# Performance work log

Hardware: AMD Instinct MI355X
Metric: run time of the kernel (lower is better)

The kernel has to match this reference:

```python
import math
import jax, jax.numpy as jnp
import numpy as np

CHUNK_LEN = 64
NUM_HEADS = 16
HIDDEN = 1024
HEAD = HIDDEN // NUM_HEADS


def setup_inputs() -> dict:
    key = jax.random.key(0)
    ks = jax.random.split(key, 8)
    B, S, C, N, L = 4, 2048, 32, 2, 128
    scale = 1.0 / math.sqrt(HIDDEN)
    return {
        "query": jax.random.normal(ks[0], (B, S, HIDDEN), jnp.float32),
        "kv": jax.random.normal(ks[1], (B, C, N, L, HIDDEN), jnp.float32),
        "Wq": jax.random.normal(ks[2], (HIDDEN, HIDDEN), jnp.float32) * scale,
        "bq": jnp.zeros((HIDDEN,), jnp.float32),
        "Wk": jax.random.normal(ks[3], (HIDDEN, HIDDEN), jnp.float32) * scale,
        "bk": jnp.zeros((HIDDEN,), jnp.float32),
        "Wv": jax.random.normal(ks[4], (HIDDEN, HIDDEN), jnp.float32) * scale,
        "bv": jnp.zeros((HIDDEN,), jnp.float32),
    }


def reference(query, kv, Wq, bq, Wk, bk, Wv, bv):
    B, S, H = query.shape
    _, C, N, L, _ = kv.shape
    # shift query right by chunk_len-1 and pad to n_chunks*chunk_len
    q = query[:, CHUNK_LEN - 1:]
    add_len = C * CHUNK_LEN - q.shape[1]
    q = jnp.pad(q, ((0, 0), (0, add_len), (0, 0)))
    q = q.reshape(B, C, CHUNK_LEN, H)
    q = (q @ Wq.T + bq).reshape(B, C, CHUNK_LEN, NUM_HEADS, HEAD)
    k = (kv @ Wk.T + bk).reshape(B, C, N, L, NUM_HEADS, HEAD)
    v = (kv @ Wv.T + bv).reshape(B, C, N, L, NUM_HEADS, HEAD)
    # scores: [B, C, heads, chunk_len, N, L]
    attn = jnp.einsum("bcihd,bcnjhd->bchinj", q, k) / math.sqrt(HEAD)
    # softmax over flattened neighbor dims (n, j)
    attn = jax.nn.softmax(attn.reshape(B, C, NUM_HEADS, CHUNK_LEN, N * L), axis=-1)
    attn = attn.reshape(B, C, NUM_HEADS, CHUNK_LEN, N, L)
    h = jnp.einsum("bchinj,bcnjhd->bcihd", attn, v).reshape(B, C * CHUNK_LEN, H)
    # shift left: prepend chunk_len-1 zeros, truncate to seq_len
    h = jnp.pad(h, ((0, 0), (CHUNK_LEN - 1, 0), (0, 0)))[:, :S]
    return h
```

## Files before the change

### kernel.cpp

```cpp
#include <hip/hip_runtime.h>
#include <stdint.h>

#define HD 1024
#define SEQ 2048
#define NC 32

typedef __bf16 bf16x4 __attribute__((ext_vector_type(4)));
typedef __bf16 bf16x8 __attribute__((ext_vector_type(8)));
typedef float f32x4 __attribute__((ext_vector_type(4)));

__device__ inline unsigned short f2bf(float f) {
  union { float f; unsigned int u; } v; v.f = f;
  unsigned int r = v.u + 0x7fffu + ((v.u >> 16) & 1u);
  return (unsigned short)(r >> 16);
}
__device__ inline unsigned int pk2bf(float a, float b) {
  return (unsigned int)f2bf(a) | ((unsigned int)f2bf(b) << 16);
}
__device__ inline bf16x8 ld_frag8(const unsigned short* p) {
  bf16x4 lo = *(const bf16x4*)p;
  bf16x4 hi = *(const bf16x4*)(p + 4);
  return __builtin_shufflevector(lo, hi, 0, 1, 2, 3, 4, 5, 6, 7);
}
__device__ inline void glds16(const unsigned short* g, unsigned short* l) {
  __builtin_amdgcn_global_load_lds(
      (const __attribute__((address_space(1))) unsigned int*)g,
      (__attribute__((address_space(3))) unsigned int*)l, 16, 0, 0);
}
__device__ inline int2 swz_bid() {
  int lin = blockIdx.y * 8 + blockIdx.x;
  int s = (lin & 7) * (int)gridDim.y + (lin >> 3);
  return make_int2(s & 7, s >> 3);
}

__global__ __launch_bounds__(256) void zero_head_kernel(float* __restrict__ out) {
  int i = (blockIdx.x * 256 + threadIdx.x) * 4;
  int b = i / 64512;
  int r = i - b * 64512;
  *(float4*)(out + (size_t)b * (SEQ * HD) + r) = make_float4(0.f, 0.f, 0.f, 0.f);
}

__global__ __launch_bounds__(256) void cvt_kernel(const float* __restrict__ in,
                                                  unsigned short* __restrict__ out, int n8) {
  int i = blockIdx.x * 256 + threadIdx.x;
  if (i < n8) {
    float4 a = ((const float4*)in)[(size_t)i * 2];
    float4 b = ((const float4*)in)[(size_t)i * 2 + 1];
    ((uint4*)out)[i] = make_uint4(pk2bf(a.x, a.y), pk2bf(a.z, a.w),
                                  pk2bf(b.x, b.y), pk2bf(b.z, b.w));
  }
}

__global__ __launch_bounds__(256) void cvt_q_kernel(const float* __restrict__ q,
                                                    unsigned short* __restrict__ out) {
  int i = blockIdx.x * 256 + threadIdx.x;
  int g = i >> 7, c8 = (i & 127) * 8;
  int b = g >> 11, tt = g & 2047;
  uint4 o = make_uint4(0, 0, 0, 0);
  if (tt < 1985) {
    const float* src = q + ((size_t)(b << 11) + tt + 63) * HD + c8;
    float4 a = *(const float4*)src;
    float4 bb = *(const float4*)(src + 4);
    o = make_uint4(pk2bf(a.x, a.y), pk2bf(a.z, a.w), pk2bf(bb.x, bb.y), pk2bf(bb.z, bb.w));
  }
  *(uint4*)(out + (size_t)g * HD + c8) = o;
}

__global__ __launch_bounds__(256, 2) void gemm_bf_kernel(
    const unsigned short* __restrict__ A, const unsigned short* __restrict__ W,
    const float* __restrict__ bias, unsigned short* __restrict__ Cout, int store_vt) {
  __shared__ unsigned short lds_a[128 * 32];
  __shared__ unsigned short lds_b[128 * 32];
  const int t = threadIdx.x;
  const int l = t & 63, w = t >> 6;
  const int wm = w >> 1, wn = w & 1;
  const int lr = l & 15, lq = l >> 4;
  const int2 bid = swz_bid();
  const size_t arow0 = (size_t)bid.y * 128;
  const size_t brow0 = (size_t)bid.x * 128;
  const int c0 = t, c1 = 256 + t;
  const unsigned short* a0 = A + (arow0 + (c0 >> 2)) * HD + (c0 & 3) * 8;
  const unsigned short* a1 = A + (arow0 + (c1 >> 2)) * HD + (c1 & 3) * 8;
  const unsigned short* b0 = W + (brow0 + (c0 >> 2)) * HD + (c0 & 3) * 8;
  const unsigned short* b1 = W + (brow0 + (c1 >> 2)) * HD + (c1 & 3) * 8;

  f32x4 acc[4][4];
  for (int i = 0; i < 4; i++)
    for (int j = 0; j < 4; j++) acc[i][j] = (f32x4){0.f, 0.f, 0.f, 0.f};

  for (int kk = 0; kk < 32; ++kk) {
    const int k0 = kk * 32;
    __syncthreads();
    glds16(a0 + k0, lds_a + c0 * 8);
    glds16(a1 + k0, lds_a + c1 * 8);
    glds16(b0 + k0, lds_b + c0 * 8);
    glds16(b1 + k0, lds_b + c1 * 8);
    __syncthreads();
    bf16x8 af[4], bfr[4];
    for (int mt = 0; mt < 4; ++mt)
      af[mt] = *(const bf16x8*)(lds_a + (wm * 64 + mt * 16 + lr) * 32 + lq * 8);
    for (int nt = 0; nt < 4; ++nt)
      bfr[nt] = *(const bf16x8*)(lds_b + (wn * 64 + nt * 16 + lr) * 32 + lq * 8);
    for (int mt = 0; mt < 4; ++mt)
      for (int nt = 0; nt < 4; ++nt)
        acc[mt][nt] = __builtin_amdgcn_mfma_f32_16x16x32_bf16(af[mt], bfr[nt], acc[mt][nt], 0, 0, 0);
  }

  if (!store_vt) {
    for (int nt = 0; nt < 4; ++nt) {
      int n = bid.x * 128 + wn * 64 + nt * 16 + lr;
      float bvv = bias[n];
      for (int mt = 0; mt < 4; ++mt) {
        size_t mbase = arow0 + wm * 64 + mt * 16 + lq * 4;
        for (int r = 0; r < 4; ++r)
          Cout[(mbase + r) * HD + n] = f2bf(acc[mt][nt][r] + bvv);
      }
    }
  } else {
    for (int nt = 0; nt < 4; ++nt) {
      int n = bid.x * 128 + wn * 64 + nt * 16 + lr;
      float bvv = bias[n];
      int h = n >> 6, d = n & 63;
      for (int mt = 0; mt < 4; ++mt) {
        size_t m0 = arow0 + wm * 64 + mt * 16 + lq * 4;
        size_t bc = m0 >> 8, j = m0 & 255;
        *(ushort4*)(Cout + ((bc * 16 + h) * 64 + d) * 256 + j) =
            make_ushort4(f2bf(acc[mt][nt][0] + bvv), f2bf(acc[mt][nt][1] + bvv),
                         f2bf(acc[mt][nt][2] + bvv), f2bf(acc[mt][nt][3] + bvv));
      }
    }
  }
}

__global__ __launch_bounds__(256, 2) void gemm_kv_kernel(
    const unsigned short* __restrict__ A, const unsigned short* __restrict__ Wk,
    const unsigned short* __restrict__ Wv, const float* __restrict__ bk,
    const float* __restrict__ bv, unsigned short* __restrict__ Kout,
    unsigned short* __restrict__ Vt) {
  __shared__ unsigned short lds_a[128 * 32];
  __shared__ unsigned short lds_k[128 * 32];
  __shared__ unsigned short lds_v[128 * 32];
  const int t = threadIdx.x;
  const int l = t & 63, w = t >> 6;
  const int wm = w >> 1, wn = w & 1;
  const int lr = l & 15, lq = l >> 4;
  const int2 bid = swz_bid();
  const size_t arow0 = (size_t)bid.y * 128;
  const size_t brow0 = (size_t)bid.x * 128;
  const int c0 = t, c1 = 256 + t;
  const unsigned short* a0 = A + (arow0 + (c0 >> 2)) * HD + (c0 & 3) * 8;
  const unsigned short* a1 = A + (arow0 + (c1 >> 2)) * HD + (c1 & 3) * 8;
  const unsigned short* k0p = Wk + (brow0 + (c0 >> 2)) * HD + (c0 & 3) * 8;
  const unsigned short* k1p = Wk + (brow0 + (c1 >> 2)) * HD + (c1 & 3) * 8;
  const unsigned short* v0p = Wv + (brow0 + (c0 >> 2)) * HD + (c0 & 3) * 8;
  const unsigned short* v1p = Wv + (brow0 + (c1 >> 2)) * HD + (c1 & 3) * 8;

  f32x4 acck[4][4], accv[4][4];
  for (int i = 0; i < 4; i++)
    for (int j = 0; j < 4; j++) {
      acck[i][j] = (f32x4){0.f, 0.f, 0.f, 0.f};
      accv[i][j] = (f32x4){0.f, 0.f, 0.f, 0.f};
    }

  for (int kk = 0; kk < 32; ++kk) {
    const int k0 = kk * 32;
    __syncthreads();
    glds16(a0 + k0, lds_a + c0 * 8);
    glds16(a1 + k0, lds_a + c1 * 8);
    glds16(k0p + k0, lds_k + c0 * 8);
    glds16(k1p + k0, lds_k + c1 * 8);
    glds16(v0p + k0, lds_v + c0 * 8);
    glds16(v1p + k0, lds_v + c1 * 8);
    __syncthreads();
    bf16x8 af[4];
    for (int mt = 0; mt < 4; ++mt)
      af[mt] = *(const bf16x8*)(lds_a + (wm * 64 + mt * 16 + lr) * 32 + lq * 8);
    {
      bf16x8 bfr[4];
      for (int nt = 0; nt < 4; ++nt)
        bfr[nt] = *(const bf16x8*)(lds_k + (wn * 64 + nt * 16 + lr) * 32 + lq * 8);
      for (int mt = 0; mt < 4; ++mt)
        for (int nt = 0; nt < 4; ++nt)
          acck[mt][nt] = __builtin_amdgcn_mfma_f32_16x16x32_bf16(af[mt], bfr[nt], acck[mt][nt], 0, 0, 0);
    }
    {
      bf16x8 bfr[4];
      for (int nt = 0; nt < 4; ++nt)
        bfr[nt] = *(const bf16x8*)(lds_v + (wn * 64 + nt * 16 + lr) * 32 + lq * 8);
      for (int mt = 0; mt < 4; ++mt)
        for (int nt = 0; nt < 4; ++nt)
          accv[mt][nt] = __builtin_amdgcn_mfma_f32_16x16x32_bf16(af[mt], bfr[nt], accv[mt][nt], 0, 0, 0);
    }
  }

  for (int nt = 0; nt < 4; ++nt) {
    int n = bid.x * 128 + wn * 64 + nt * 16 + lr;
    float bvv = bk[n];
    for (int mt = 0; mt < 4; ++mt) {
      size_t mbase = arow0 + wm * 64 + mt * 16 + lq * 4;
      for (int r = 0; r < 4; ++r)
        Kout[(mbase + r) * HD + n] = f2bf(acck[mt][nt][r] + bvv);
    }
  }
  for (int nt = 0; nt < 4; ++nt) {
    int n = bid.x * 128 + wn * 64 + nt * 16 + lr;
    float bvv = bv[n];
    int h = n >> 6, d = n & 63;
    for (int mt = 0; mt < 4; ++mt) {
      size_t m0 = arow0 + wm * 64 + mt * 16 + lq * 4;
      size_t bc = m0 >> 8, j = m0 & 255;
      *(ushort4*)(Vt + ((bc * 16 + h) * 64 + d) * 256 + j) =
          make_ushort4(f2bf(accv[mt][nt][0] + bvv), f2bf(accv[mt][nt][1] + bvv),
                       f2bf(accv[mt][nt][2] + bvv), f2bf(accv[mt][nt][3] + bvv));
    }
  }
}

__global__ __launch_bounds__(256, 2) void gemm_f32_kernel(
    const float* __restrict__ A, const float* __restrict__ W,
    const float* __restrict__ bias, unsigned short* __restrict__ Cout,
    int store_vt, int qremap) {
  __shared__ unsigned short lds_a[128 * 32];
  __shared__ unsigned short lds_b[128 * 32];
  const int t = threadIdx.x;
  const int l = t & 63, w = t >> 6;
  const int wm = w >> 1, wn = w & 1;
  const int lr = l & 15, lq = l >> 4;
  const size_t arow0 = (size_t)blockIdx.y * 128;
  const size_t brow0 = (size_t)blockIdx.x * 128;

  f32x4 acc[4][4];
  for (int i = 0; i < 4; i++)
    for (int j = 0; j < 4; j++) acc[i][j] = (f32x4){0.f, 0.f, 0.f, 0.f};

  for (int kk = 0; kk < 32; ++kk) {
    const int k0 = kk * 32;
    uint4 av[2], bv[2];
    for (int p = 0; p < 2; ++p) {
      int chunk = p * 256 + t;
      int row = chunk >> 2, c8 = (chunk & 3) * 8;
      size_t grow = arow0 + row;
      bool valid = true;
      const float* srcA;
      if (qremap) {
        int bb = (int)(grow >> 11), tt = (int)(grow & 2047);
        valid = tt < 1985;
        srcA = A + ((size_t)(bb << 11) + tt + 63) * HD + k0 + c8;
      } else {
        srcA = A + grow * HD + k0 + c8;
      }
      if (valid) {
        float4 x = *(const float4*)srcA, y = *(const float4*)(srcA + 4);
        av[p] = make_uint4(pk2bf(x.x, x.y), pk2bf(x.z, x.w), pk2bf(y.x, y.y), pk2bf(y.z, y.w));
      } else av[p] = make_uint4(0, 0, 0, 0);
      const float* srcB = W + (brow0 + row) * HD + k0 + c8;
      float4 x = *(const float4*)srcB, y = *(const float4*)(srcB + 4);
      bv[p] = make_uint4(pk2bf(x.x, x.y), pk2bf(x.z, x.w), pk2bf(y.x, y.y), pk2bf(y.z, y.w));
    }
    __syncthreads();
    for (int p = 0; p < 2; ++p) {
      int chunk = p * 256 + t;
      *(uint4*)(lds_a + chunk * 8) = av[p];
      *(uint4*)(lds_b + chunk * 8) = bv[p];
    }
    __syncthreads();
    bf16x8 af[4], bfr[4];
    for (int mt = 0; mt < 4; ++mt)
      af[mt] = *(const bf16x8*)(lds_a + (wm * 64 + mt * 16 + lr) * 32 + lq * 8);
    for (int nt = 0; nt < 4; ++nt)
      bfr[nt] = *(const bf16x8*)(lds_b + (wn * 64 + nt * 16 + lr) * 32 + lq * 8);
    for (int mt = 0; mt < 4; ++mt)
      for (int nt = 0; nt < 4; ++nt)
        acc[mt][nt] = __builtin_amdgcn_mfma_f32_16x16x32_bf16(af[mt], bfr[nt], acc[mt][nt], 0, 0, 0);
  }

  if (!store_vt) {
    for (int nt = 0; nt < 4; ++nt) {
      int n = blockIdx.x * 128 + wn * 64 + nt * 16 + lr;
      float bvv = bias[n];
      for (int mt = 0; mt < 4; ++mt) {
        size_t mbase = arow0 + wm * 64 + mt * 16 + lq * 4;
        for (int r = 0; r < 4; ++r)
          Cout[(mbase + r) * HD + n] = f2bf(acc[mt][nt][r] + bvv);
      }
    }
  } else {
    for (int nt = 0; nt < 4; ++nt) {
      int n = blockIdx.x * 128 + wn * 64 + nt * 16 + lr;
      float bvv = bias[n];
      int h = n >> 6, d = n & 63;
      for (int mt = 0; mt < 4; ++mt) {
        size_t m0 = arow0 + wm * 64 + mt * 16 + lq * 4;
        size_t bc = m0 >> 8, j = m0 & 255;
        *(ushort4*)(Cout + ((bc * 16 + h) * 64 + d) * 256 + j) =
            make_ushort4(f2bf(acc[mt][nt][0] + bvv), f2bf(acc[mt][nt][1] + bvv),
                         f2bf(acc[mt][nt][2] + bvv), f2bf(acc[mt][nt][3] + bvv));
      }
    }
  }
}

#define QK_STRIDE 68
#define P_STRIDE 260

__global__ __launch_bounds__(256, 3) void attn_kernel(
    const unsigned short* __restrict__ Qp, const unsigned short* __restrict__ Kp,
    const unsigned short* __restrict__ Vt, float* __restrict__ out) {
  __shared__ unsigned short q_s[64 * QK_STRIDE];
  __shared__ unsigned short k_s[256 * QK_STRIDE];
  const int t = threadIdx.x;
  const int l = t & 63, w = t >> 6;
  const int lr = l & 15, lq = l >> 4;
  const int bid = blockIdx.x;
  const int head = bid & 15, cc = (bid >> 4) & 31, b = bid >> 9;
  const size_t qrow0 = (size_t)(b * NC + cc) * 64;
  const size_t kvrow0 = (size_t)(b * NC + cc) * 256;
  const int hcol = head * 64;
  const unsigned short* vbase = Vt + ((size_t)((b * NC + cc) * 16 + head) * 64) * 256;

  for (int p = 0; p < 4; ++p) {
    int chunk = p * 256 + t;
    int row = chunk >> 4, c4 = (chunk & 15) * 4;
    *(uint2*)(q_s + row * QK_STRIDE + c4) = *(const uint2*)(Qp + (qrow0 + row) * HD + hcol + c4);
  }
  for (int p = 0; p < 16; ++p) {
    int chunk = p * 256 + t;
    int row = chunk >> 4, c4 = (chunk & 15) * 4;
    *(uint2*)(k_s + row * QK_STRIDE + c4) = *(const uint2*)(Kp + (kvrow0 + row) * HD + hcol + c4);
  }
  __syncthreads();

  bf16x8 qa0 = ld_frag8(q_s + (w * 16 + lr) * QK_STRIDE + lq * 8);
  bf16x8 qa1 = ld_frag8(q_s + (w * 16 + lr) * QK_STRIDE + 32 + lq * 8);
  f32x4 sc[16];
  for (int nt = 0; nt < 16; ++nt) {
    bf16x8 kb0 = ld_frag8(k_s + (nt * 16 + lr) * QK_STRIDE + lq * 8);
    bf16x8 kb1 = ld_frag8(k_s + (nt * 16 + lr) * QK_STRIDE + 32 + lq * 8);
    f32x4 a = (f32x4){0.f, 0.f, 0.f, 0.f};
    a = __builtin_amdgcn_mfma_f32_16x16x32_bf16(qa0, kb0, a, 0, 0, 0);
    a = __builtin_amdgcn_mfma_f32_16x16x32_bf16(qa1, kb1, a, 0, 0, 0);
    sc[nt] = a;
  }
  float mrow[4] = {-1e30f, -1e30f, -1e30f, -1e30f};
  for (int nt = 0; nt < 16; ++nt)
    for (int r = 0; r < 4; ++r) mrow[r] = fmaxf(mrow[r], sc[nt][r]);
  for (int off = 1; off < 16; off <<= 1)
    for (int r = 0; r < 4; ++r) mrow[r] = fmaxf(mrow[r], __shfl_xor(mrow[r], off, 16));
  float srow[4] = {0.f, 0.f, 0.f, 0.f};
  const float cexp = 0.18033688011112042f;
  for (int nt = 0; nt < 16; ++nt)
    for (int r = 0; r < 4; ++r) {
      float p = exp2f((sc[nt][r] - mrow[r]) * cexp);
      sc[nt][r] = p;
      srow[r] += p;
    }
  for (int off = 1; off < 16; off <<= 1)
    for (int r = 0; r < 4; ++r) srow[r] += __shfl_xor(srow[r], off, 16);

  __syncthreads();

  for (int nt = 0; nt < 16; ++nt)
    for (int r = 0; r < 4; ++r)
      k_s[(w * 16 + lq * 4 + r) * P_STRIDE + nt * 16 + lr] = f2bf(sc[nt][r]);

  f32x4 o[4];
  for (int i = 0; i < 4; ++i) o[i] = (f32x4){0.f, 0.f, 0.f, 0.f};
  for (int ks = 0; ks < 8; ++ks) {
    bf16x8 pa = ld_frag8(k_s + (w * 16 + lr) * P_STRIDE + ks * 32 + lq * 8);
    for (int nt2 = 0; nt2 < 4; ++nt2) {
      bf16x8 vb = *(const bf16x8*)(vbase + (size_t)(nt2 * 16 + lr) * 256 + ks * 32 + lq * 8);
      o[nt2] = __builtin_amdgcn_mfma_f32_16x16x32_bf16(pa, vb, o[nt2], 0, 0, 0);
    }
  }

  for (int r = 0; r < 4; ++r) {
    int strip = w * 16 + lq * 4 + r;
    int trow = cc * 64 + strip;
    if (trow < 1985) {
      size_t orow = (size_t)b * SEQ + trow + 63;
      float inv = 1.0f / srow[r];
      for (int nt2 = 0; nt2 < 4; ++nt2)
        out[orow * HD + hcol + nt2 * 16 + lr] = o[nt2][r] * inv;
    }
  }
}

extern "C" void kernel_launch(void* const* d_in, const int* in_sizes, int n_in,
                              void* d_out, int out_size, void* d_ws, size_t ws_size,
                              hipStream_t stream) {
  (void)in_sizes; (void)n_in; (void)out_size;
  const float* query = (const float*)d_in[0];
  const float* kv    = (const float*)d_in[1];
  const float* Wq    = (const float*)d_in[2];
  const float* bq    = (const float*)d_in[3];
  const float* Wk    = (const float*)d_in[4];
  const float* bk    = (const float*)d_in[5];
  const float* Wv    = (const float*)d_in[6];
  const float* bv    = (const float*)d_in[7];
  float* out = (float*)d_out;

  unsigned short* Qp  = (unsigned short*)d_ws;
  unsigned short* Kp  = Qp + (size_t)8192 * 1024;
  unsigned short* Vt  = Kp + (size_t)32768 * 1024;
  unsigned short* Qbf = Vt + (size_t)32768 * 1024;
  unsigned short* KVb = Qbf + (size_t)8192 * 1024;
  unsigned short* Wqb = KVb + (size_t)32768 * 1024;
  unsigned short* Wkb = Wqb + (size_t)1024 * 1024;
  unsigned short* Wvb = Wkb + (size_t)1024 * 1024;
  const size_t need = ((size_t)8192 * 1024 * 2 + (size_t)32768 * 1024 * 2 + (size_t)1024 * 1024 * 3) * 2;
  const bool big = ws_size >= need;

  zero_head_kernel<<<dim3(252), dim3(256), 0, stream>>>(out);
  if (big) {
    cvt_q_kernel<<<dim3(4096), dim3(256), 0, stream>>>(query, Qbf);
    cvt_kernel<<<dim3(16384), dim3(256), 0, stream>>>(kv, KVb, 4194304);
    cvt_kernel<<<dim3(512), dim3(256), 0, stream>>>(Wq, Wqb, 131072);
    cvt_kernel<<<dim3(512), dim3(256), 0, stream>>>(Wk, Wkb, 131072);
    cvt_kernel<<<dim3(512), dim3(256), 0, stream>>>(Wv, Wvb, 131072);
    gemm_bf_kernel<<<dim3(8, 64), dim3(256), 0, stream>>>(Qbf, Wqb, bq, Qp, 0);
    gemm_kv_kernel<<<dim3(8, 256), dim3(256), 0, stream>>>(KVb, Wkb, Wvb, bk, bv, Kp, Vt);
  } else {
    gemm_f32_kernel<<<dim3(8, 64), dim3(256), 0, stream>>>(query, Wq, bq, Qp, 0, 1);
    gemm_f32_kernel<<<dim3(8, 256), dim3(256), 0, stream>>>(kv, Wk, bk, Kp, 0, 0);
    gemm_f32_kernel<<<dim3(8, 256), dim3(256), 0, stream>>>(kv, Wv, bv, Vt, 1, 0);
  }
  attn_kernel<<<dim3(2048), dim3(256), 0, stream>>>(Qp, Kp, Vt, out);
}
```

Measured before the change: 484.4 us.

## Double-buffer GEMMs, swizzle LDS, fuse kv conversion into KV GEMM, widen attn loads

Both projection GEMMs now double-buffer their LDS tiles, so the next K-slice is loaded while MFMAs run on the current one, with one barrier per iteration instead of two. The LDS layout is XOR-swizzled to avoid bank conflicts on fragment reads. The KV GEMM reads fp32 kv directly and converts it to bf16 in registers before writing LDS, which removes the separate kv conversion pass and its large intermediate buffer. The attention kernel loads Q/K with 16-byte vectors and a padded stride of 72. The cost is double the LDS and more registers, which may lower occupancy.

```diff
diff --git a/kernel.cpp b/kernel.cpp
--- a/kernel.cpp
+++ b/kernel.cpp
@@ -31,6 +31,13 @@
   int lin = blockIdx.y * 8 + blockIdx.x;
   int s = (lin & 7) * (int)gridDim.y + (lin >> 3);
   return make_int2(s & 7, s >> 3);
+}
+__device__ inline int inv_swz(int pc) {
+  int b2 = (pc >> 2) & 1, b3 = (pc >> 3) & 1, b4 = (pc >> 4) & 1;
+  return pc ^ (b2 ^ b4) ^ (b3 << 1) ^ (b4 << 2);
+}
+__device__ inline int swz_rd(int row, int lq) {
+  return (((row << 2) | lq) ^ (row & 7)) << 3;
 }
 
 __global__ __launch_bounds__(256) void zero_head_kernel(float* __restrict__ out) {
@@ -66,11 +73,11 @@
   *(uint4*)(out + (size_t)g * HD + c8) = o;
 }
 
-__global__ __launch_bounds__(256, 2) void gemm_bf_kernel(
+__global__ __launch_bounds__(256, 2) void gemm_q_kernel(
     const unsigned short* __restrict__ A, const unsigned short* __restrict__ W,
-    const float* __restrict__ bias, unsigned short* __restrict__ Cout, int store_vt) {
-  __shared__ unsigned short lds_a[128 * 32];
-  __shared__ unsigned short lds_b[128 * 32];
+    const float* __restrict__ bias, unsigned short* __restrict__ Cout) {
+  __shared__ unsigned short lds_a[2][4096];
+  __shared__ unsigned short lds_b[2][4096];
   const int t = threadIdx.x;
   const int l = t & 63, w = t >> 6;
   const int wm = w >> 1, wn = w & 1;
@@ -78,68 +85,62 @@
   const int2 bid = swz_bid();
   const size_t arow0 = (size_t)bid.y * 128;
   const size_t brow0 = (size_t)bid.x * 128;
-  const int c0 = t, c1 = 256 + t;
-  const unsigned short* a0 = A + (arow0 + (c0 >> 2)) * HD + (c0 & 3) * 8;
-  const unsigned short* a1 = A + (arow0 + (c1 >> 2)) * HD + (c1 & 3) * 8;
-  const unsigned short* b0 = W + (brow0 + (c0 >> 2)) * HD + (c0 & 3) * 8;
-  const unsigned short* b1 = W + (brow0 + (c1 >> 2)) * HD + (c1 & 3) * 8;
+  const int lc = inv_swz(t);
+  const int r0 = lc >> 2, c8 = (lc & 3) * 8;
+  const unsigned short* a0 = A + (arow0 + r0) * HD + c8;
+  const unsigned short* a1 = a0 + 64 * HD;
+  const unsigned short* b0 = W + (brow0 + r0) * HD + c8;
+  const unsigned short* b1 = b0 + 64 * HD;
 
   f32x4 acc[4][4];
   for (int i = 0; i < 4; i++)
     for (int j = 0; j < 4; j++) acc[i][j] = (f32x4){0.f, 0.f, 0.f, 0.f};
 
-  for (int kk = 0; kk < 32; ++kk) {
-    const int k0 = kk * 32;
-    __syncthreads();
-    glds16(a0 + k0, lds_a + c0 * 8);
-    glds16(a1 + k0, lds_a + c1 * 8);
-    glds16(b0 + k0, lds_b + c0 * 8);
-    glds16(b1 + k0, lds_b + c1 * 8);
-    __syncthreads();
+  auto stage = [&](int buf, int k0) {
+    glds16(a0 + k0, lds_a[buf] + t * 8);
+    glds16(a1 + k0, lds_a[buf] + 2048 + t * 8);
+    glds16(b0 + k0, lds_b[buf] + t * 8);
+    glds16(b1 + k0, lds_b[buf] + 2048 + t * 8);
+  };
+  auto compute = [&](int buf) {
     bf16x8 af[4], bfr[4];
     for (int mt = 0; mt < 4; ++mt)
-      af[mt] = *(const bf16x8*)(lds_a + (wm * 64 + mt * 16 + lr) * 32 + lq * 8);
+      af[mt] = *(const bf16x8*)(lds_a[buf] + swz_rd(wm * 64 + mt * 16 + lr, lq));
     for (int nt = 0; nt < 4; ++nt)
-      bfr[nt] = *(const bf16x8*)(lds_b + (wn * 64 + nt * 16 + lr) * 32 + lq * 8);
+      bfr[nt] = *(const bf16x8*)(lds_b[buf] + swz_rd(wn * 64 + nt * 16 + lr, lq));
     for (int mt = 0; mt < 4; ++mt)
       for (int nt = 0; nt < 4; ++nt)
         acc[mt][nt] = __builtin_amdgcn_mfma_f32_16x16x32_bf16(af[mt], bfr[nt], acc[mt][nt], 0, 0, 0);
-  }
-
-  if (!store_vt) {
-    for (int nt = 0; nt < 4; ++nt) {
-      int n = bid.x * 128 + wn * 64 + nt * 16 + lr;
-      float bvv = bias[n];
-      for (int mt = 0; mt < 4; ++mt) {
-        size_t mbase = arow0 + wm * 64 + mt * 16 + lq * 4;
-        for (int r = 0; r < 4; ++r)
-          Cout[(mbase + r) * HD + n] = f2bf(acc[mt][nt][r] + bvv);
-      }
-    }
-  } else {
-    for (int nt = 0; nt < 4; ++nt) {
-      int n = bid.x * 128 + wn * 64 + nt * 16 + lr;
-      float bvv = bias[n];
-      int h = n >> 6, d = n & 63;
-      for (int mt = 0; mt < 4; ++mt) {
-        size_t m0 = arow0 + wm * 64 + mt * 16 + lq * 4;
-        size_t bc = m0 >> 8, j = m0 & 255;
-        *(ushort4*)(Cout + ((bc * 16 + h) * 64 + d) * 256 + j) =
-            make_ushort4(f2bf(acc[mt][nt][0] + bvv), f2bf(acc[mt][nt][1] + bvv),
-                         f2bf(acc[mt][nt][2] + bvv), f2bf(acc[mt][nt][3] + bvv));
-      }
+  };
+
+  stage(0, 0);
+  __syncthreads();
+  for (int kk = 0; kk < 31; ++kk) {
+    stage((kk & 1) ^ 1, (kk + 1) * 32);
+    compute(kk & 1);
+    __syncthreads();
+  }
+  compute(1);
+
+  for (int nt = 0; nt < 4; ++nt) {
+    int n = bid.x * 128 + wn * 64 + nt * 16 + lr;
+    float bvv = bias[n];
+    for (int mt = 0; mt < 4; ++mt) {
+      size_t mbase = arow0 + wm * 64 + mt * 16 + lq * 4;
+      for (int r = 0; r < 4; ++r)
+        Cout[(mbase + r) * HD + n] = f2bf(acc[mt][nt][r] + bvv);
     }
   }
 }
 
 __global__ __launch_bounds__(256, 2) void gemm_kv_kernel(
-    const unsigned short* __restrict__ A, const unsigned short* __restrict__ Wk,
+    const float* __restrict__ A, const unsigned short* __restrict__ Wk,
     const unsigned short* __restrict__ Wv, const float* __restrict__ bk,
     const float* __restrict__ bv, unsigned short* __restrict__ Kout,
     unsigned short* __restrict__ Vt) {
-  __shared__ unsigned short lds_a[128 * 32];
-  __shared__ unsigned short lds_k[128 * 32];
-  __shared__ unsigned short lds_v[128 * 32];
+  __shared__ unsigned short lds_a[2][4096];
+  __shared__ unsigned short lds_k[2][4096];
+  __shared__ unsigned short lds_v[2][4096];
   const int t = threadIdx.x;
   const int l = t & 63, w = t >> 6;
   const int wm = w >> 1, wn = w & 1;
@@ -147,13 +148,14 @@
   const int2 bid = swz_bid();
   const size_t arow0 = (size_t)bid.y * 128;
   const size_t brow0 = (size_t)bid.x * 128;
-  const int c0 = t, c1 = 256 + t;
-  const unsigned short* a0 = A + (arow0 + (c0 >> 2)) * HD + (c0 & 3) * 8;
-  const unsigned short* a1 = A + (arow0 + (c1 >> 2)) * HD + (c1 & 3) * 8;
-  const unsigned short* k0p = Wk + (brow0 + (c0 >> 2)) * HD + (c0 & 3) * 8;
-  const unsigned short* k1p = Wk + (brow0 + (c1 >> 2)) * HD + (c1 & 3) * 8;
-  const unsigned short* v0p = Wv + (brow0 + (c0 >> 2)) * HD + (c0 & 3) * 8;
-  const unsigned short* v1p = Wv + (brow0 + (c1 >> 2)) * HD + (c1 & 3) * 8;
+  const int lc = inv_swz(t);
+  const int r0 = lc >> 2, c8 = (lc & 3) * 8;
+  const float* aF0 = A + (arow0 + r0) * HD + c8;
+  const float* aF1 = aF0 + (size_t)64 * HD;
+  const unsigned short* kp0 = Wk + (brow0 + r0) * HD + c8;
+  const unsigned short* kp1 = kp0 + 64 * HD;
+  const unsigned short* vp0 = Wv + (brow0 + r0) * HD + c8;
+  const unsigned short* vp1 = vp0 + 64 * HD;
 
   f32x4 acck[4][4], accv[4][4];
   for (int i = 0; i < 4; i++)
@@ -162,23 +164,31 @@
       accv[i][j] = (f32x4){0.f, 0.f, 0.f, 0.f};
     }
 
-  for (int kk = 0; kk < 32; ++kk) {
-    const int k0 = kk * 32;
-    __syncthreads();
-    glds16(a0 + k0, lds_a + c0 * 8);
-    glds16(a1 + k0, lds_a + c1 * 8);
-    glds16(k0p + k0, lds_k + c0 * 8);
-    glds16(k1p + k0, lds_k + c1 * 8);
-    glds16(v0p + k0, lds_v + c0 * 8);
-    glds16(v1p + k0, lds_v + c1 * 8);
-    __syncthreads();
+  float4 fa0, fa1, fb0, fb1;
+  auto loadA = [&](int k0) {
+    fa0 = *(const float4*)(aF0 + k0); fa1 = *(const float4*)(aF0 + k0 + 4);
+    fb0 = *(const float4*)(aF1 + k0); fb1 = *(const float4*)(aF1 + k0 + 4);
+  };
+  auto gldsW = [&](int buf, int k0) {
+    glds16(kp0 + k0, lds_k[buf] + t * 8);
+    glds16(kp1 + k0, lds_k[buf] + 2048 + t * 8);
+    glds16(vp0 + k0, lds_v[buf] + t * 8);
+    glds16(vp1 + k0, lds_v[buf] + 2048 + t * 8);
+  };
+  auto writeA = [&](int buf) {
+    *(uint4*)(lds_a[buf] + t * 8) =
+        make_uint4(pk2bf(fa0.x, fa0.y), pk2bf(fa0.z, fa0.w), pk2bf(fa1.x, fa1.y), pk2bf(fa1.z, fa1.w));
+    *(uint4*)(lds_a[buf] + 2048 + t * 8) =
+        make_uint4(pk2bf(fb0.x, fb0.y), pk2bf(fb0.z, fb0.w), pk2bf(fb1.x, fb1.y), pk2bf(fb1.z, fb1.w));
+  };
+  auto compute = [&](int buf) {
     bf16x8 af[4];
     for (int mt = 0; mt < 4; ++mt)
-      af[mt] = *(const bf16x8*)(lds_a + (wm * 64 + mt * 16 + lr) * 32 + lq * 8);
+      af[mt] = *(const bf16x8*)(lds_a[buf] + swz_rd(wm * 64 + mt * 16 + lr, lq));
     {
       bf16x8 bfr[4];
       for (int nt = 0; nt < 4; ++nt)
-        bfr[nt] = *(const bf16x8*)(lds_k + (wn * 64 + nt * 16 + lr) * 32 + lq * 8);
+        bfr[nt] = *(const bf16x8*)(lds_k[buf] + swz_rd(wn * 64 + nt * 16 + lr, lq));
       for (int mt = 0; mt < 4; ++mt)
         for (int nt = 0; nt < 4; ++nt)
           acck[mt][nt] = __builtin_amdgcn_mfma_f32_16x16x32_bf16(af[mt], bfr[nt], acck[mt][nt], 0, 0, 0);
@@ -186,12 +196,25 @@
     {
       bf16x8 bfr[4];
       for (int nt = 0; nt < 4; ++nt)
-        bfr[nt] = *(const bf16x8*)(lds_v + (wn * 64 + nt * 16 + lr) * 32 + lq * 8);
+        bfr[nt] = *(const bf16x8*)(lds_v[buf] + swz_rd(wn * 64 + nt * 16 + lr, lq));
       for (int mt = 0; mt < 4; ++mt)
         for (int nt = 0; nt < 4; ++nt)
           accv[mt][nt] = __builtin_amdgcn_mfma_f32_16x16x32_bf16(af[mt], bfr[nt], accv[mt][nt], 0, 0, 0);
     }
-  }
+  };
+
+  loadA(0); gldsW(0, 0); writeA(0);
+  __syncthreads();
+  for (int kk = 0; kk < 31; ++kk) {
+    const int cur = kk & 1;
+    const int k0n = (kk + 1) * 32;
+    loadA(k0n);
+    gldsW(cur ^ 1, k0n);
+    compute(cur);
+    writeA(cur ^ 1);
+    __syncthreads();
+  }
+  compute(1);
 
   for (int nt = 0; nt < 4; ++nt) {
     int n = bid.x * 128 + wn * 64 + nt * 16 + lr;
@@ -300,7 +323,7 @@
   }
 }
 
-#define QK_STRIDE 68
+#define QK_STRIDE 72
 #define P_STRIDE 260
 
 __global__ __launch_bounds__(256, 3) void attn_kernel(
@@ -318,15 +341,15 @@
   const int hcol = head * 64;
   const unsigned short* vbase = Vt + ((size_t)((b * NC + cc) * 16 + head) * 64) * 256;
 
-  for (int p = 0; p < 4; ++p) {
+  for (int p = 0; p < 2; ++p) {
     int chunk = p * 256 + t;
-    int row = chunk >> 4, c4 = (chunk & 15) * 4;
-    *(uint2*)(q_s + row * QK_STRIDE + c4) = *(const uint2*)(Qp + (qrow0 + row) * HD + hcol + c4);
-  }
-  for (int p = 0; p < 16; ++p) {
+    int row = chunk >> 3, c8 = (chunk & 7) * 8;
+    *(uint4*)(q_s + row * QK_STRIDE + c8) = *(const uint4*)(Qp + (qrow0 + row) * HD + hcol + c8);
+  }
+  for (int p = 0; p < 8; ++p) {
     int chunk = p * 256 + t;
-    int row = chunk >> 4, c4 = (chunk & 15) * 4;
-    *(uint2*)(k_s + row * QK_STRIDE + c4) = *(const uint2*)(Kp + (kvrow0 + row) * HD + hcol + c4);
+    int row = chunk >> 3, c8 = (chunk & 7) * 8;
+    *(uint4*)(k_s + row * QK_STRIDE + c8) = *(const uint4*)(Kp + (kvrow0 + row) * HD + hcol + c8);
   }
   __syncthreads();
 
@@ -413,12 +436,11 @@
   zero_head_kernel<<<dim3(252), dim3(256), 0, stream>>>(out);
   if (big) {
     cvt_q_kernel<<<dim3(4096), dim3(256), 0, stream>>>(query, Qbf);
-    cvt_kernel<<<dim3(16384), dim3(256), 0, stream>>>(kv, KVb, 4194304);
     cvt_kernel<<<dim3(512), dim3(256), 0, stream>>>(Wq, Wqb, 131072);
     cvt_kernel<<<dim3(512), dim3(256), 0, stream>>>(Wk, Wkb, 131072);
     cvt_kernel<<<dim3(512), dim3(256), 0, stream>>>(Wv, Wvb, 131072);
-    gemm_bf_kernel<<<dim3(8, 64), dim3(256), 0, stream>>>(Qbf, Wqb, bq, Qp, 0);
-    gemm_kv_kernel<<<dim3(8, 256), dim3(256), 0, stream>>>(KVb, Wkb, Wvb, bk, bv, Kp, Vt);
+    gemm_q_kernel<<<dim3(8, 64), dim3(256), 0, stream>>>(Qbf, Wqb, bq, Qp);
+    gemm_kv_kernel<<<dim3(8, 256), dim3(256), 0, stream>>>(kv, Wkb, Wvb, bk, bv, Kp, Vt);
   } else {
     gemm_f32_kernel<<<dim3(8, 64), dim3(256), 0, stream>>>(query, Wq, bq, Qp, 0, 1);
     gemm_f32_kernel<<<dim3(8, 256), dim3(256), 0, stream>>>(kv, Wk, bk, Kp, 0, 0);
```

Result: slower. 523.7 us (+8.1%).

## Widen GEMM K-tile with XOR-swizzled LDS, merge prep kernels, prefetch V in attention

Applied to the files above, without the earlier changes.

The GEMM kernels now stage 64-wide K tiles in LDS using an XOR swizzle, so the K loop runs half as many iterations and has fewer barriers, and fragment reads avoid bank conflicts. The zeroing and Q conversion kernels are merged into one launch, and the three weight conversions into another, to cut launch overhead. The attention kernel loads Q and K with 16-byte vectors, pads the LDS stride, double-buffers V fragments from global memory, and raises wave priority around the MFMA sections. In exchange, LDS use per GEMM block grows, which could lower occupancy, and register pressure rises in attention.

```diff
diff --git a/kernel.cpp b/kernel.cpp
--- a/kernel.cpp
+++ b/kernel.cpp
@@ -32,12 +32,37 @@
   int s = (lin & 7) * (int)gridDim.y + (lin >> 3);
   return make_int2(s & 7, s >> 3);
 }
+__device__ inline int swz64(int row, int j) { return (row * 8 + (j ^ (row & 7))) * 8; }
 
 __global__ __launch_bounds__(256) void zero_head_kernel(float* __restrict__ out) {
   int i = (blockIdx.x * 256 + threadIdx.x) * 4;
   int b = i / 64512;
   int r = i - b * 64512;
   *(float4*)(out + (size_t)b * (SEQ * HD) + r) = make_float4(0.f, 0.f, 0.f, 0.f);
+}
+
+__global__ __launch_bounds__(256) void prep_q_kernel(const float* __restrict__ q,
+                                                     unsigned short* __restrict__ out,
+                                                     float* __restrict__ oz) {
+  int bid = blockIdx.x;
+  if (bid < 252) {
+    int i = (bid * 256 + threadIdx.x) * 4;
+    int b = i / 64512;
+    int r = i - b * 64512;
+    *(float4*)(oz + (size_t)b * (SEQ * HD) + r) = make_float4(0.f, 0.f, 0.f, 0.f);
+    return;
+  }
+  int i = (bid - 252) * 256 + threadIdx.x;
+  int g = i >> 7, c8 = (i & 127) * 8;
+  int b = g >> 11, tt = g & 2047;
+  uint4 o = make_uint4(0, 0, 0, 0);
+  if (tt < 1985) {
+    const float* src = q + ((size_t)(b << 11) + tt + 63) * HD + c8;
+    float4 a = *(const float4*)src;
+    float4 bb = *(const float4*)(src + 4);
+    o = make_uint4(pk2bf(a.x, a.y), pk2bf(a.z, a.w), pk2bf(bb.x, bb.y), pk2bf(bb.z, bb.w));
+  }
+  *(uint4*)(out + (size_t)g * HD + c8) = o;
 }
 
 __global__ __launch_bounds__(256) void cvt_kernel(const float* __restrict__ in,
@@ -51,26 +76,25 @@
   }
 }
 
-__global__ __launch_bounds__(256) void cvt_q_kernel(const float* __restrict__ q,
-                                                    unsigned short* __restrict__ out) {
-  int i = blockIdx.x * 256 + threadIdx.x;
-  int g = i >> 7, c8 = (i & 127) * 8;
-  int b = g >> 11, tt = g & 2047;
-  uint4 o = make_uint4(0, 0, 0, 0);
-  if (tt < 1985) {
-    const float* src = q + ((size_t)(b << 11) + tt + 63) * HD + c8;
-    float4 a = *(const float4*)src;
-    float4 bb = *(const float4*)(src + 4);
-    o = make_uint4(pk2bf(a.x, a.y), pk2bf(a.z, a.w), pk2bf(bb.x, bb.y), pk2bf(bb.z, bb.w));
-  }
-  *(uint4*)(out + (size_t)g * HD + c8) = o;
-}
-
-__global__ __launch_bounds__(256, 2) void gemm_bf_kernel(
+__global__ __launch_bounds__(256) void cvt_w3_kernel(const float* __restrict__ Wq,
+                                                     const float* __restrict__ Wk,
+                                                     const float* __restrict__ Wv,
+                                                     unsigned short* __restrict__ dst) {
+  int bid = blockIdx.x;
+  int which = bid >> 9;
+  int i = (bid & 511) * 256 + threadIdx.x;
+  const float* src = which == 0 ? Wq : (which == 1 ? Wk : Wv);
+  float4 a = ((const float4*)src)[(size_t)i * 2];
+  float4 b = ((const float4*)src)[(size_t)i * 2 + 1];
+  ((uint4*)(dst + (size_t)which * 1048576))[i] =
+      make_uint4(pk2bf(a.x, a.y), pk2bf(a.z, a.w), pk2bf(b.x, b.y), pk2bf(b.z, b.w));
+}
+
+__global__ __launch_bounds__(256, 2) void gemm_q_kernel(
     const unsigned short* __restrict__ A, const unsigned short* __restrict__ W,
-    const float* __restrict__ bias, unsigned short* __restrict__ Cout, int store_vt) {
-  __shared__ unsigned short lds_a[128 * 32];
-  __shared__ unsigned short lds_b[128 * 32];
+    const float* __restrict__ bias, unsigned short* __restrict__ Cout) {
+  __shared__ unsigned short lds_a[128 * 64];
+  __shared__ unsigned short lds_b[128 * 64];
   const int t = threadIdx.x;
   const int l = t & 63, w = t >> 6;
   const int wm = w >> 1, wn = w & 1;
@@ -78,56 +102,47 @@
   const int2 bid = swz_bid();
   const size_t arow0 = (size_t)bid.y * 128;
   const size_t brow0 = (size_t)bid.x * 128;
-  const int c0 = t, c1 = 256 + t;
-  const unsigned short* a0 = A + (arow0 + (c0 >> 2)) * HD + (c0 & 3) * 8;
-  const unsigned short* a1 = A + (arow0 + (c1 >> 2)) * HD + (c1 & 3) * 8;
-  const unsigned short* b0 = W + (brow0 + (c0 >> 2)) * HD + (c0 & 3) * 8;
-  const unsigned short* b1 = W + (brow0 + (c1 >> 2)) * HD + (c1 & 3) * 8;
+  int pr[4], pco[4];
+#pragma unroll
+  for (int p = 0; p < 4; ++p) {
+    int pc = p * 256 + t;
+    pr[p] = pc >> 3;
+    pco[p] = ((pc & 7) ^ (pr[p] & 7)) * 8;
+  }
 
   f32x4 acc[4][4];
   for (int i = 0; i < 4; i++)
     for (int j = 0; j < 4; j++) acc[i][j] = (f32x4){0.f, 0.f, 0.f, 0.f};
 
-  for (int kk = 0; kk < 32; ++kk) {
-    const int k0 = kk * 32;
-    __syncthreads();
-    glds16(a0 + k0, lds_a + c0 * 8);
-    glds16(a1 + k0, lds_a + c1 * 8);
-    glds16(b0 + k0, lds_b + c0 * 8);
-    glds16(b1 + k0, lds_b + c1 * 8);
-    __syncthreads();
-    bf16x8 af[4], bfr[4];
-    for (int mt = 0; mt < 4; ++mt)
-      af[mt] = *(const bf16x8*)(lds_a + (wm * 64 + mt * 16 + lr) * 32 + lq * 8);
-    for (int nt = 0; nt < 4; ++nt)
-      bfr[nt] = *(const bf16x8*)(lds_b + (wn * 64 + nt * 16 + lr) * 32 + lq * 8);
-    for (int mt = 0; mt < 4; ++mt)
+  for (int kk = 0; kk < 16; ++kk) {
+    const int k0 = kk * 64;
+    __syncthreads();
+#pragma unroll
+    for (int p = 0; p < 4; ++p) {
+      glds16(A + (arow0 + pr[p]) * HD + k0 + pco[p], lds_a + (p * 256 + t) * 8);
+      glds16(W + (brow0 + pr[p]) * HD + k0 + pco[p], lds_b + (p * 256 + t) * 8);
+    }
+    __syncthreads();
+#pragma unroll
+    for (int h = 0; h < 2; ++h) {
+      bf16x8 af[4], bfr[4];
+      for (int mt = 0; mt < 4; ++mt)
+        af[mt] = *(const bf16x8*)(lds_a + swz64(wm * 64 + mt * 16 + lr, h * 4 + lq));
       for (int nt = 0; nt < 4; ++nt)
-        acc[mt][nt] = __builtin_amdgcn_mfma_f32_16x16x32_bf16(af[mt], bfr[nt], acc[mt][nt], 0, 0, 0);
-  }
-
-  if (!store_vt) {
-    for (int nt = 0; nt < 4; ++nt) {
-      int n = bid.x * 128 + wn * 64 + nt * 16 + lr;
-      float bvv = bias[n];
-      for (int mt = 0; mt < 4; ++mt) {
-        size_t mbase = arow0 + wm * 64 + mt * 16 + lq * 4;
-        for (int r = 0; r < 4; ++r)
-          Cout[(mbase + r) * HD + n] = f2bf(acc[mt][nt][r] + bvv);
-      }
-    }
-  } else {
-    for (int nt = 0; nt < 4; ++nt) {
-      int n = bid.x * 128 + wn * 64 + nt * 16 + lr;
-      float bvv = bias[n];
-      int h = n >> 6, d = n & 63;
-      for (int mt = 0; mt < 4; ++mt) {
-        size_t m0 = arow0 + wm * 64 + mt * 16 + lq * 4;
-        size_t bc = m0 >> 8, j = m0 & 255;
-        *(ushort4*)(Cout + ((bc * 16 + h) * 64 + d) * 256 + j) =
-            make_ushort4(f2bf(acc[mt][nt][0] + bvv), f2bf(acc[mt][nt][1] + bvv),
-                         f2bf(acc[mt][nt][2] + bvv), f2bf(acc[mt][nt][3] + bvv));
-      }
+        bfr[nt] = *(const bf16x8*)(lds_b + swz64(wn * 64 + nt * 16 + lr, h * 4 + lq));
+      for (int mt = 0; mt < 4; ++mt)
+        for (int nt = 0; nt < 4; ++nt)
+          acc[mt][nt] = __builtin_amdgcn_mfma_f32_16x16x32_bf16(af[mt], bfr[nt], acc[mt][nt], 0, 0, 0);
+    }
+  }
+
+  for (int nt = 0; nt < 4; ++nt) {
+    int n = bid.x * 128 + wn * 64 + nt * 16 + lr;
+    float bvv = bias[n];
+    for (int mt = 0; mt < 4; ++mt) {
+      size_t mbase = arow0 + wm * 64 + mt * 16 + lq * 4;
+      for (int r = 0; r < 4; ++r)
+        Cout[(mbase + r) * HD + n] = f2bf(acc[mt][nt][r] + bvv);
     }
   }
 }
@@ -137,9 +152,9 @@
     const unsigned short* __restrict__ Wv, const float* __restrict__ bk,
     const float* __restrict__ bv, unsigned short* __restrict__ Kout,
     unsigned short* __restrict__ Vt) {
-  __shared__ unsigned short lds_a[128 * 32];
-  __shared__ unsigned short lds_k[128 * 32];
-  __shared__ unsigned short lds_v[128 * 32];
+  __shared__ unsigned short lds_a[128 * 64];
+  __shared__ unsigned short lds_k[128 * 64];
+  __shared__ unsigned short lds_v[128 * 64];
   const int t = threadIdx.x;
   const int l = t & 63, w = t >> 6;
   const int wm = w >> 1, wn = w & 1;
@@ -147,13 +162,13 @@
   const int2 bid = swz_bid();
   const size_t arow0 = (size_t)bid.y * 128;
   const size_t brow0 = (size_t)bid.x * 128;
-  const int c0 = t, c1 = 256 + t;
-  const unsigned short* a0 = A + (arow0 + (c0 >> 2)) * HD + (c0 & 3) * 8;
-  const unsigned short* a1 = A + (arow0 + (c1 >> 2)) * HD + (c1 & 3) * 8;
-  const unsigned short* k0p = Wk + (brow0 + (c0 >> 2)) * HD + (c0 & 3) * 8;
-  const unsigned short* k1p = Wk + (brow0 + (c1 >> 2)) * HD + (c1 & 3) * 8;
-  const unsigned short* v0p = Wv + (brow0 + (c0 >> 2)) * HD + (c0 & 3) * 8;
-  const unsigned short* v1p = Wv + (brow0 + (c1 >> 2)) * HD + (c1 & 3) * 8;
+  int pr[4], pco[4];
+#pragma unroll
+  for (int p = 0; p < 4; ++p) {
+    int pc = p * 256 + t;
+    pr[p] = pc >> 3;
+    pco[p] = ((pc & 7) ^ (pr[p] & 7)) * 8;
+  }
 
   f32x4 acck[4][4], accv[4][4];
   for (int i = 0; i < 4; i++)
@@ -162,34 +177,37 @@
       accv[i][j] = (f32x4){0.f, 0.f, 0.f, 0.f};
     }
 
-  for (int kk = 0; kk < 32; ++kk) {
-    const int k0 = kk * 32;
-    __syncthreads();
-    glds16(a0 + k0, lds_a + c0 * 8);
-    glds16(a1 + k0, lds_a + c1 * 8);
-    glds16(k0p + k0, lds_k + c0 * 8);
-    glds16(k1p + k0, lds_k + c1 * 8);
-    glds16(v0p + k0, lds_v + c0 * 8);
-    glds16(v1p + k0, lds_v + c1 * 8);
-    __syncthreads();
-    bf16x8 af[4];
-    for (int mt = 0; mt < 4; ++mt)
-      af[mt] = *(const bf16x8*)(lds_a + (wm * 64 + mt * 16 + lr) * 32 + lq * 8);
-    {
-      bf16x8 bfr[4];
-      for (int nt = 0; nt < 4; ++nt)
-        bfr[nt] = *(const bf16x8*)(lds_k + (wn * 64 + nt * 16 + lr) * 32 + lq * 8);
+  for (int kk = 0; kk < 16; ++kk) {
+    const int k0 = kk * 64;
+    __syncthreads();
+#pragma unroll
+    for (int p = 0; p < 4; ++p) {
+      glds16(A + (arow0 + pr[p]) * HD + k0 + pco[p], lds_a + (p * 256 + t) * 8);
+      glds16(Wk + (brow0 + pr[p]) * HD + k0 + pco[p], lds_k + (p * 256 + t) * 8);
+      glds16(Wv + (brow0 + pr[p]) * HD + k0 + pco[p], lds_v + (p * 256 + t) * 8);
+    }
+    __syncthreads();
+#pragma unroll
+    for (int h = 0; h < 2; ++h) {
+      bf16x8 af[4];
       for (int mt = 0; mt < 4; ++mt)
+        af[mt] = *(const bf16x8*)(lds_a + swz64(wm * 64 + mt * 16 + lr, h * 4 + lq));
+      {
+        bf16x8 bfr[4];
         for (int nt = 0; nt < 4; ++nt)
-          acck[mt][nt] = __builtin_amdgcn_mfma_f32_16x16x32_bf16(af[mt], bfr[nt], acck[mt][nt], 0, 0, 0);
-    }
-    {
-      bf16x8 bfr[4];
-      for (int nt = 0; nt < 4; ++nt)
-        bfr[nt] = *(const bf16x8*)(lds_v + (wn * 64 + nt * 16 + lr) * 32 + lq * 8);
-      for (int mt = 0; mt < 4; ++mt)
+          bfr[nt] = *(const bf16x8*)(lds_k + swz64(wn * 64 + nt * 16 + lr, h * 4 + lq));
+        for (int mt = 0; mt < 4; ++mt)
+          for (int nt = 0; nt < 4; ++nt)
+            acck[mt][nt] = __builtin_amdgcn_mfma_f32_16x16x32_bf16(af[mt], bfr[nt], acck[mt][nt], 0, 0, 0);
+      }
+      {
+        bf16x8 bfr[4];
         for (int nt = 0; nt < 4; ++nt)
-          accv[mt][nt] = __builtin_amdgcn_mfma_f32_16x16x32_bf16(af[mt], bfr[nt], accv[mt][nt], 0, 0, 0);
+          bfr[nt] = *(const bf16x8*)(lds_v + swz64(wn * 64 + nt * 16 + lr, h * 4 + lq));
+        for (int mt = 0; mt < 4; ++mt)
+          for (int nt = 0; nt < 4; ++nt)
+            accv[mt][nt] = __builtin_amdgcn_mfma_f32_16x16x32_bf16(af[mt], bfr[nt], accv[mt][nt], 0, 0, 0);
+      }
     }
   }
 
@@ -300,7 +318,7 @@
   }
 }
 
-#define QK_STRIDE 68
+#define QK_STRIDE 72
 #define P_STRIDE 260
 
 __global__ __launch_bounds__(256, 3) void attn_kernel(
@@ -318,21 +336,22 @@
   const int hcol = head * 64;
   const unsigned short* vbase = Vt + ((size_t)((b * NC + cc) * 16 + head) * 64) * 256;
 
-  for (int p = 0; p < 4; ++p) {
+  for (int p = 0; p < 2; ++p) {
     int chunk = p * 256 + t;
-    int row = chunk >> 4, c4 = (chunk & 15) * 4;
-    *(uint2*)(q_s + row * QK_STRIDE + c4) = *(const uint2*)(Qp + (qrow0 + row) * HD + hcol + c4);
-  }
-  for (int p = 0; p < 16; ++p) {
+    int row = chunk >> 3, c8 = (chunk & 7) * 8;
+    *(uint4*)(q_s + row * QK_STRIDE + c8) = *(const uint4*)(Qp + (qrow0 + row) * HD + hcol + c8);
+  }
+  for (int p = 0; p < 8; ++p) {
     int chunk = p * 256 + t;
-    int row = chunk >> 4, c4 = (chunk & 15) * 4;
-    *(uint2*)(k_s + row * QK_STRIDE + c4) = *(const uint2*)(Kp + (kvrow0 + row) * HD + hcol + c4);
+    int row = chunk >> 3, c8 = (chunk & 7) * 8;
+    *(uint4*)(k_s + row * QK_STRIDE + c8) = *(const uint4*)(Kp + (kvrow0 + row) * HD + hcol + c8);
   }
   __syncthreads();
 
   bf16x8 qa0 = ld_frag8(q_s + (w * 16 + lr) * QK_STRIDE + lq * 8);
   bf16x8 qa1 = ld_frag8(q_s + (w * 16 + lr) * QK_STRIDE + 32 + lq * 8);
   f32x4 sc[16];
+  __builtin_amdgcn_s_setprio(1);
   for (int nt = 0; nt < 16; ++nt) {
     bf16x8 kb0 = ld_frag8(k_s + (nt * 16 + lr) * QK_STRIDE + lq * 8);
     bf16x8 kb1 = ld_frag8(k_s + (nt * 16 + lr) * QK_STRIDE + 32 + lq * 8);
@@ -341,6 +360,7 @@
     a = __builtin_amdgcn_mfma_f32_16x16x32_bf16(qa1, kb1, a, 0, 0, 0);
     sc[nt] = a;
   }
+  __builtin_amdgcn_s_setprio(0);
   float mrow[4] = {-1e30f, -1e30f, -1e30f, -1e30f};
   for (int nt = 0; nt < 16; ++nt)
     for (int r = 0; r < 4; ++r) mrow[r] = fmaxf(mrow[r], sc[nt][r]);
@@ -357,6 +377,11 @@
   for (int off = 1; off < 16; off <<= 1)
     for (int r = 0; r < 4; ++r) srow[r] += __shfl_xor(srow[r], off, 16);
 
+  bf16x8 va[4];
+#pragma unroll
+  for (int nt2 = 0; nt2 < 4; ++nt2)
+    va[nt2] = *(const bf16x8*)(vbase + (size_t)(nt2 * 16 + lr) * 256 + lq * 8);
+
   __syncthreads();
 
   for (int nt = 0; nt < 16; ++nt)
@@ -365,12 +390,29 @@
 
   f32x4 o[4];
   for (int i = 0; i < 4; ++i) o[i] = (f32x4){0.f, 0.f, 0.f, 0.f};
-  for (int ks = 0; ks < 8; ++ks) {
+  bf16x8 vbuf[4];
+#pragma unroll
+  for (int ks = 0; ks < 8; ks += 2) {
+#pragma unroll
+    for (int nt2 = 0; nt2 < 4; ++nt2)
+      vbuf[nt2] = *(const bf16x8*)(vbase + (size_t)(nt2 * 16 + lr) * 256 + (ks + 1) * 32 + lq * 8);
     bf16x8 pa = ld_frag8(k_s + (w * 16 + lr) * P_STRIDE + ks * 32 + lq * 8);
-    for (int nt2 = 0; nt2 < 4; ++nt2) {
-      bf16x8 vb = *(const bf16x8*)(vbase + (size_t)(nt2 * 16 + lr) * 256 + ks * 32 + lq * 8);
-      o[nt2] = __builtin_amdgcn_mfma_f32_16x16x32_bf16(pa, vb, o[nt2], 0, 0, 0);
-    }
+    __builtin_amdgcn_s_setprio(1);
+#pragma unroll
+    for (int nt2 = 0; nt2 < 4; ++nt2)
+      o[nt2] = __builtin_amdgcn_mfma_f32_16x16x32_bf16(pa, va[nt2], o[nt2], 0, 0, 0);
+    __builtin_amdgcn_s_setprio(0);
+    if (ks + 2 < 8) {
+#pragma unroll
+      for (int nt2 = 0; nt2 < 4; ++nt2)
+        va[nt2] = *(const bf16x8*)(vbase + (size_t)(nt2 * 16 + lr) * 256 + (ks + 2) * 32 + lq * 8);
+    }
+    bf16x8 pb = ld_frag8(k_s + (w * 16 + lr) * P_STRIDE + (ks + 1) * 32 + lq * 8);
+    __builtin_amdgcn_s_setprio(1);
+#pragma unroll
+    for (int nt2 = 0; nt2 < 4; ++nt2)
+      o[nt2] = __builtin_amdgcn_mfma_f32_16x16x32_bf16(pb, vbuf[nt2], o[nt2], 0, 0, 0);
+    __builtin_amdgcn_s_setprio(0);
   }
 
   for (int r = 0; r < 4; ++r) {
@@ -405,21 +447,18 @@
   unsigned short* Qbf = Vt + (size_t)32768 * 1024;
   unsigned short* KVb = Qbf + (size_t)8192 * 1024;
   unsigned short* Wqb = KVb + (size_t)32768 * 1024;
-  unsigned short* Wkb = Wqb + (size_t)1024 * 1024;
-  unsigned short* Wvb = Wkb + (size_t)1024 * 1024;
   const size_t need = ((size_t)8192 * 1024 * 2 + (size_t)32768 * 1024 * 2 + (size_t)1024 * 1024 * 3) * 2;
   const bool big = ws_size >= need;
 
-  zero_head_kernel<<<dim3(252), dim3(256), 0, stream>>>(out);
   if (big) {
-    cvt_q_kernel<<<dim3(4096), dim3(256), 0, stream>>>(query, Qbf);
+    prep_q_kernel<<<dim3(4348), dim3(256), 0, stream>>>(query, Qbf, out);
+    cvt_w3_kernel<<<dim3(1536), dim3(256), 0, stream>>>(Wq, Wk, Wv, Wqb);
     cvt_kernel<<<dim3(16384), dim3(256), 0, stream>>>(kv, KVb, 4194304);
-    cvt_kernel<<<dim3(512), dim3(256), 0, stream>>>(Wq, Wqb, 131072);
-    cvt_kernel<<<dim3(512), dim3(256), 0, stream>>>(Wk, Wkb, 131072);
-    cvt_kernel<<<dim3(512), dim3(256), 0, stream>>>(Wv, Wvb, 131072);
-    gemm_bf_kernel<<<dim3(8, 64), dim3(256), 0, stream>>>(Qbf, Wqb, bq, Qp, 0);
-    gemm_kv_kernel<<<dim3(8, 256), dim3(256), 0, stream>>>(KVb, Wkb, Wvb, bk, bv, Kp, Vt);
+    gemm_q_kernel<<<dim3(8, 64), dim3(256), 0, stream>>>(Qbf, Wqb, bq, Qp);
+    gemm_kv_kernel<<<dim3(8, 256), dim3(256), 0, stream>>>(KVb, Wqb + (size_t)1048576,
+                                                           Wqb + (size_t)2097152, bk, bv, Kp, Vt);
   } else {
+    zero_head_kernel<<<dim3(252), dim3(256), 0, stream>>>(out);
     gemm_f32_kernel<<<dim3(8, 64), dim3(256), 0, stream>>>(query, Wq, bq, Qp, 0, 1);
     gemm_f32_kernel<<<dim3(8, 256), dim3(256), 0, stream>>>(kv, Wk, bk, Kp, 0, 0);
     gemm_f32_kernel<<<dim3(8, 256), dim3(256), 0, stream>>>(kv, Wv, bv, Vt, 1, 0);
```

Measured after the change: 461.5 us. 4.7% less time.
